# Kernel optimization log

Measured on AMD Instinct MI355X. Metric: run time of the kernel, lower is better.

Reference implementation:

```python
import jax, jax.numpy as jnp
import numpy as np
from jax import lax

K = 3          # dcn kernel size
KK = K * K     # 9 taps
PAD = 1


def _conv(x, w, b, pad):
    y = lax.conv_general_dilated(
        x, w, window_strides=(1, 1), padding=[(pad, pad), (pad, pad)],
        dimension_numbers=("NCHW", "OIHW", "NCHW"))
    return y + b[None, :, None, None]


def _bilinear_gather(x, py, px):
    """Zero-padded bilinear sampling.
    x: [B,C,Hin,Win]; py,px: [B,KK,H,W] float sample coords.
    returns [B,C,KK,H,W]."""
    B, C, Hin, Win = x.shape
    y0 = jnp.floor(py)
    x0 = jnp.floor(px)
    ly = py - y0   # frac weights
    lx = px - x0
    xf = x.reshape(B, C, Hin * Win)

    def corner(yc, xc, w):
        valid = (yc >= 0) & (yc <= Hin - 1) & (xc >= 0) & (xc <= Win - 1)
        yi = jnp.clip(yc, 0, Hin - 1).astype(jnp.int32)
        xi = jnp.clip(xc, 0, Win - 1).astype(jnp.int32)
        idx = yi * Win + xi                              # [B,KK,H,W]
        vals = jax.vmap(lambda f, i: jnp.take(f, i, axis=1))(xf, idx)  # [B,C,KK,H,W]
        return vals * (w * valid.astype(x.dtype))[:, None]

    out = corner(y0,     x0,     (1 - ly) * (1 - lx))
    out = out + corner(y0,     x0 + 1, (1 - ly) * lx)
    out = out + corner(y0 + 1, x0,     ly * (1 - lx))
    out = out + corner(y0 + 1, x0 + 1, ly * lx)
    return out


def _forward(x, conv1_w, conv1_b, off_w, off_b, dcn_w, dcn_b):
    # features: Conv2d(1,3,3,s1,p1) + ReLU + MaxPool(3,2)
    h = jax.nn.relu(_conv(x, conv1_w, conv1_b, pad=1))
    h = lax.reduce_window(h, -jnp.inf, lax.max,
                          window_dimensions=(1, 1, 3, 3),
                          window_strides=(1, 1, 2, 2), padding="VALID")
    B, C, H, W = h.shape

    # DCNv2: conv_offset_mask -> (dy, dx, sigmoid mask)
    om = _conv(h, off_w, off_b, pad=PAD)          # [B, 3*KK, H, W]
    dy = om[:, :KK]
    dx = om[:, KK:2 * KK]
    mask = jax.nn.sigmoid(om[:, 2 * KK:])         # [B, KK, H, W]

    # base sampling grid (stride 1, pad 1, dilation 1)
    ky = (jnp.arange(KK) // K).astype(h.dtype)    # kernel row of each tap
    kx = (jnp.arange(KK) % K).astype(h.dtype)
    hh = jnp.arange(H, dtype=h.dtype)
    ww = jnp.arange(W, dtype=h.dtype)
    py = hh[None, None, :, None] - PAD + ky[None, :, None, None] + dy
    px = ww[None, None, None, :] - PAD + kx[None, :, None, None] + dx

    sampled = _bilinear_gather(h, py, px)          # [B,C,KK,H,W]
    sampled = sampled * mask[:, None]              # modulation
    out = jnp.einsum("bckhw,ock->bohw", sampled,
                     dcn_w.reshape(dcn_w.shape[0], C, KK))
    return out + dcn_b[None, :, None, None]


def setup_inputs() -> dict:
    key = jax.random.key(0)
    ks = jax.random.split(key, 7)
    x = jax.random.normal(ks[0], (32, 1, 512, 512), dtype=jnp.float32)
    conv1_w = jax.random.normal(ks[1], (3, 1, 3, 3), dtype=jnp.float32) * 0.5
    conv1_b = jnp.zeros((3,), dtype=jnp.float32)
    # offset/mask conv: 3*KK = 27 output channels; small init so offsets are modest
    off_w = jax.random.normal(ks[2], (3 * KK, 3, 3, 3), dtype=jnp.float32) * 0.01
    off_b = jax.random.normal(ks[3], (3 * KK,), dtype=jnp.float32) * 0.01
    dcn_w = jax.random.normal(ks[4], (3, 3, 3, 3), dtype=jnp.float32) * 0.1
    dcn_b = jnp.zeros((3,), dtype=jnp.float32)
    return {"x": x, "conv1_w": conv1_w, "conv1_b": conv1_b,
            "off_w": off_w, "off_b": off_b, "dcn_w": dcn_w, "dcn_b": dcn_b}


def reference(x, conv1_w, conv1_b, off_w, off_b, dcn_w, dcn_b):
    return _forward(x, conv1_w, conv1_b, off_w, off_b, dcn_w, dcn_b)
```

## Files before the change

### kernel.cpp

```cpp
#include <hip/hip_runtime.h>
#include <math.h>

#define B_  32
#define H0  512
#define W0  512
#define Hh  255
#define Wh  255
#define HP  259

typedef __attribute__((ext_vector_type(8))) short    bf16x8;
typedef __attribute__((ext_vector_type(4))) float    f32x4;
typedef __attribute__((ext_vector_type(4))) unsigned int u32x4;

static __device__ __forceinline__ unsigned int f2bf(float f) {
    unsigned int u = __float_as_uint(f);
    return (u + 0x7FFFu + ((u >> 16) & 1u)) >> 16;
}
static __device__ __forceinline__ float bflo(unsigned int u) { return __uint_as_float(u << 16); }
static __device__ __forceinline__ float bfhi(unsigned int u) { return __uint_as_float(u & 0xFFFF0000u); }

__global__ __launch_bounds__(256) void conv_pool_kernel(
    const float* __restrict__ x,
    const float* __restrict__ w,
    const float* __restrict__ bias,
    uint2* __restrict__ hp)
{
    __shared__ float sx[35][36];
    __shared__ float sc[33 * 100];
    const int b  = blockIdx.z;
    const int i0 = blockIdx.y * 16;
    const int j0 = blockIdx.x * 16;
    const int tx = threadIdx.x, ty = threadIdx.y;
    const int tid = ty * 16 + tx;

    const float* xb = x + b * (H0 * W0);
    for (int t = tid; t < 35 * 35; t += 256) {
        int r = t / 35, c = t - r * 35;
        int gr = 2 * i0 - 1 + r;
        int gc = 2 * j0 - 1 + c;
        float v = 0.f;
        if ((unsigned)gr < (unsigned)H0 && (unsigned)gc < (unsigned)W0) v = xb[gr * W0 + gc];
        sx[r][c] = v;
    }
    __syncthreads();

    float w0[9], w1[9], w2[9];
#pragma unroll
    for (int t = 0; t < 9; ++t) { w0[t] = w[t]; w1[t] = w[9 + t]; w2[t] = w[18 + t]; }
    const float b0 = bias[0], b1 = bias[1], b2 = bias[2];

    for (int t = tid; t < 33 * 33; t += 256) {
        int r = t / 33, c = t - r * 33;
        float s0 = b0, s1 = b1, s2 = b2;
#pragma unroll
        for (int ky = 0; ky < 3; ++ky) {
#pragma unroll
            for (int kx = 0; kx < 3; ++kx) {
                float v = sx[r + ky][c + kx];
                s0 = fmaf(w0[ky * 3 + kx], v, s0);
                s1 = fmaf(w1[ky * 3 + kx], v, s1);
                s2 = fmaf(w2[ky * 3 + kx], v, s2);
            }
        }
        float* p = &sc[r * 100 + c * 3];
        p[0] = s0; p[1] = s1; p[2] = s2;
    }
    __syncthreads();

    const int i = i0 + ty, j = j0 + tx;
    if (i >= Hh || j >= Wh) return;

    float m0 = -1e30f, m1 = -1e30f, m2 = -1e30f;
#pragma unroll
    for (int pr = 0; pr < 3; ++pr) {
#pragma unroll
        for (int pc = 0; pc < 3; ++pc) {
            const float* p = &sc[(2 * ty + pr) * 100 + (2 * tx + pc) * 3];
            m0 = fmaxf(m0, p[0]);
            m1 = fmaxf(m1, p[1]);
            m2 = fmaxf(m2, p[2]);
        }
    }
    m0 = fmaxf(m0, 0.f); m1 = fmaxf(m1, 0.f); m2 = fmaxf(m2, 0.f);

    uint2 v;
    v.x = f2bf(m0) | (f2bf(m1) << 16);
    v.y = f2bf(m2);
    hp[(b * HP + i + 2) * HP + (j + 2)] = v;
}

__global__ __launch_bounds__(256, 5) void dcn_kernel(
    const uint2* __restrict__ hp,
    const float* __restrict__ off_w,
    const float* __restrict__ off_b,
    const float* __restrict__ dcn_w,
    const float* __restrict__ dcn_b,
    float* __restrict__ out)
{
    __shared__ __align__(16) char smem[256 * 28 * 4];
    float* om_s = (float*)smem;

    const int y   = blockIdx.x;
    const int b   = blockIdx.y;
    const int tid = threadIdx.x;
    const int x   = tid;

    const uint2* hb = hp + b * (HP * HP);

    {
        unsigned short* Bm = (unsigned short*)(smem + 16384);
        for (int idx = tid; idx < 1024; idx += 256) {
            int n = idx >> 5, k = idx & 31;
            float v = (n < 27 && k < 27) ? off_w[n * 27 + k] : 0.f;
            Bm[n * 32 + k] = (unsigned short)f2bf(v);
        }
    }

    unsigned int L[9], Hv[9];
#pragma unroll
    for (int ky = 0; ky < 3; ++ky) {
        const unsigned int rbase = (unsigned int)(y + 1 + ky) * HP + (unsigned int)(x + 1);
#pragma unroll
        for (int kx = 0; kx < 3; ++kx) {
            uint2 v = hb[rbase + kx];
            L[ky * 3 + kx]  = v.x;
            Hv[ky * 3 + kx] = v.y;
        }
    }

    {
        unsigned int T[16];
        T[0]  = (L[0] & 0xFFFFu) | (L[1] << 16);
        T[1]  = (L[2] & 0xFFFFu) | (L[3] << 16);
        T[2]  = (L[4] & 0xFFFFu) | (L[5] << 16);
        T[3]  = (L[6] & 0xFFFFu) | (L[7] << 16);
        T[4]  = (L[8] & 0xFFFFu) | (L[0] & 0xFFFF0000u);
        T[5]  = (L[1] >> 16) | (L[2] & 0xFFFF0000u);
        T[6]  = (L[3] >> 16) | (L[4] & 0xFFFF0000u);
        T[7]  = (L[5] >> 16) | (L[6] & 0xFFFF0000u);
        T[8]  = (L[7] >> 16) | (L[8] & 0xFFFF0000u);
        T[9]  = (Hv[0] & 0xFFFFu) | (Hv[1] << 16);
        T[10] = (Hv[2] & 0xFFFFu) | (Hv[3] << 16);
        T[11] = (Hv[4] & 0xFFFFu) | (Hv[5] << 16);
        T[12] = (Hv[6] & 0xFFFFu) | (Hv[7] << 16);
        T[13] = (Hv[8] & 0xFFFFu);
        T[14] = 0u;
        T[15] = 0u;
#pragma unroll
        for (int c4 = 0; c4 < 4; ++c4) {
            u32x4 v = { T[c4 * 4 + 0], T[c4 * 4 + 1], T[c4 * 4 + 2], T[c4 * 4 + 3] };
            *(u32x4*)(smem + (c4 * 256 + tid) * 16) = v;
        }
    }
    __syncthreads();

    {
        const int wave = tid >> 6, lane = tid & 63;
        const int lrow = lane & 15, lchunk = lane >> 4;
        const short* As = (const short*)smem;
        const short* Bs = (const short*)(smem + 16384);

        bf16x8 afr[4];
#pragma unroll
        for (int m = 0; m < 4; ++m)
            afr[m] = *(const bf16x8*)(As + (lchunk * 256 + wave * 64 + m * 16 + lrow) * 8);
        bf16x8 bfr[2];
#pragma unroll
        for (int nt = 0; nt < 2; ++nt)
            bfr[nt] = *(const bf16x8*)(Bs + ((nt * 16 + lrow) * 32 + lchunk * 8));

        f32x4 acc[4][2];
#pragma unroll
        for (int m = 0; m < 4; ++m)
#pragma unroll
            for (int nt = 0; nt < 2; ++nt) {
                f32x4 z = {0.f, 0.f, 0.f, 0.f};
                acc[m][nt] = __builtin_amdgcn_mfma_f32_16x16x32_bf16(afr[m], bfr[nt], z, 0, 0, 0);
            }
        __syncthreads();

#pragma unroll
        for (int m = 0; m < 4; ++m)
#pragma unroll
            for (int nt = 0; nt < 2; ++nt) {
                const int n = nt * 16 + lrow;
                if (n < 27) {
                    const int pxb = wave * 64 + m * 16 + lchunk * 4;
                    om_s[(pxb + 0) * 28 + n] = acc[m][nt][0];
                    om_s[(pxb + 1) * 28 + n] = acc[m][nt][1];
                    om_s[(pxb + 2) * 28 + n] = acc[m][nt][2];
                    om_s[(pxb + 3) * 28 + n] = acc[m][nt][3];
                }
            }
    }
    __syncthreads();

    f32x4 o4[7];
    {
        const f32x4* omv = (const f32x4*)(om_s + x * 28);
#pragma unroll
        for (int j = 0; j < 7; ++j) o4[j] = omv[j];
    }

    float outv0 = dcn_b[0], outv1 = dcn_b[1], outv2 = dcn_b[2];
    const float yf = (float)y, xf = (float)x;

#pragma unroll
    for (int k = 0; k < 9; ++k) {
        const float dy  = o4[k >> 2][k & 3]               + off_b[k];
        const float dxx = o4[(k + 9) >> 2][(k + 9) & 3]   + off_b[9 + k];
        const float zm  = o4[(k + 18) >> 2][(k + 18) & 3] + off_b[18 + k];
        const float msk = __builtin_amdgcn_rcpf(1.f + __expf(-zm));

        const float py = yf + (float)(k / 3 - 1) + dy;
        const float px = xf + (float)(k % 3 - 1) + dxx;

        const float y0f = floorf(py), x0f = floorf(px);
        const float ly = py - y0f, lx = px - x0f;
        int iy = (int)y0f, ix = (int)x0f;
        iy = min(max(iy, -2), 255);
        ix = min(max(ix, -2), 255);

        const unsigned int idx = (unsigned int)(iy + 2) * HP + (unsigned int)(ix + 2);
        const uint2 aAA = hb[idx];
        const uint2 aAB = hb[idx + 1];
        const uint2 aBA = hb[idx + HP];
        const uint2 aBB = hb[idx + HP + 1];

        const float my1 = ly * msk;
        const float my0 = msk - my1;
        const float lx1 = 1.f - lx;
        const float w00 = my0 * lx1, w01 = my0 * lx;
        const float w10 = my1 * lx1, w11 = my1 * lx;

        const float s0 = w00 * bflo(aAA.x) + w01 * bflo(aAB.x) + w10 * bflo(aBA.x) + w11 * bflo(aBB.x);
        const float s1 = w00 * bfhi(aAA.x) + w01 * bfhi(aAB.x) + w10 * bfhi(aBA.x) + w11 * bfhi(aBB.x);
        const float s2 = w00 * bflo(aAA.y) + w01 * bflo(aAB.y) + w10 * bflo(aBA.y) + w11 * bflo(aBB.y);

        outv0 = fmaf(dcn_w[0 * 27 + 0 * 9 + k], s0, outv0);
        outv0 = fmaf(dcn_w[0 * 27 + 1 * 9 + k], s1, outv0);
        outv0 = fmaf(dcn_w[0 * 27 + 2 * 9 + k], s2, outv0);
        outv1 = fmaf(dcn_w[1 * 27 + 0 * 9 + k], s0, outv1);
        outv1 = fmaf(dcn_w[1 * 27 + 1 * 9 + k], s1, outv1);
        outv1 = fmaf(dcn_w[1 * 27 + 2 * 9 + k], s2, outv1);
        outv2 = fmaf(dcn_w[2 * 27 + 0 * 9 + k], s0, outv2);
        outv2 = fmaf(dcn_w[2 * 27 + 1 * 9 + k], s1, outv2);
        outv2 = fmaf(dcn_w[2 * 27 + 2 * 9 + k], s2, outv2);
    }

    if (x < Wh) {
        const int hwsz = Hh * Wh;
        const int o = (b * 3) * hwsz + y * Wh + x;
        out[o]            = outv0;
        out[o + hwsz]     = outv1;
        out[o + 2 * hwsz] = outv2;
    }
}

extern "C" void kernel_launch(void* const* d_in, const int* in_sizes, int n_in,
                              void* d_out, int out_size, void* d_ws, size_t ws_size,
                              hipStream_t stream) {
    const float* x       = (const float*)d_in[0];
    const float* conv1_w = (const float*)d_in[1];
    const float* conv1_b = (const float*)d_in[2];
    const float* off_w   = (const float*)d_in[3];
    const float* off_b   = (const float*)d_in[4];
    const float* dcn_w   = (const float*)d_in[5];
    const float* dcn_b   = (const float*)d_in[6];
    float* out = (float*)d_out;
    uint2* hp  = (uint2*)d_ws;

    hipMemsetAsync(d_ws, 0, (size_t)B_ * HP * HP * sizeof(uint2), stream);

    conv_pool_kernel<<<dim3(16, 16, B_), dim3(16, 16), 0, stream>>>(x, conv1_w, conv1_b, hp);
    dcn_kernel<<<dim3(Hh, B_), 256, 0, stream>>>(hp, off_w, off_b, dcn_w, dcn_b, out);
}
```

Before: 81.51 us.

## Replace full workspace memset with border-only zeroing, fold bias into MFMA, vectorize gathers

Removes the full-buffer hipMemsetAsync and instead zeroes only the two-pixel padding ring of the pooled feature map, using an extra row of blocks in the conv/pool kernel. The offset-conv bias is folded into the MFMA by adding a constant-1 input column and a bias row in the weight tile. The four corner loads of the bilinear sampling become two 16-byte loads, and the pooling max is rewritten as a flat expression. The border-only zeroing depends on every interior cell being written by conv_pool on each call, and the bias now passes through bf16 rounding.

```diff
diff --git a/kernel.cpp b/kernel.cpp
--- a/kernel.cpp
+++ b/kernel.cpp
@@ -25,13 +25,32 @@
     const float* __restrict__ bias,
     uint2* __restrict__ hp)
 {
+    const int b = blockIdx.z;
+    const int tx = threadIdx.x, ty = threadIdx.y;
+    const int tid = ty * 16 + tx;
+
+    if (blockIdx.y == 16) {
+        uint2* hpb = hp + b * (HP * HP);
+        const int gid = blockIdx.x * 256 + tid;
+        if (gid < 2072) {
+            int r, c;
+            if (gid < 1036) {
+                int rr = gid / 259; c = gid - rr * 259;
+                r = rr + (rr >= 2 ? 255 : 0);
+            } else {
+                int u = gid - 1036;
+                int cc = u / 259; r = u - cc * 259;
+                c = cc + (cc >= 2 ? 255 : 0);
+            }
+            hpb[r * HP + c] = make_uint2(0u, 0u);
+        }
+        return;
+    }
+
     __shared__ float sx[35][36];
     __shared__ float sc[33 * 100];
-    const int b  = blockIdx.z;
     const int i0 = blockIdx.y * 16;
     const int j0 = blockIdx.x * 16;
-    const int tx = threadIdx.x, ty = threadIdx.y;
-    const int tid = ty * 16 + tx;
 
     const float* xb = x + b * (H0 * W0);
     for (int t = tid; t < 35 * 35; t += 256) {
@@ -70,17 +89,13 @@
     const int i = i0 + ty, j = j0 + tx;
     if (i >= Hh || j >= Wh) return;
 
-    float m0 = -1e30f, m1 = -1e30f, m2 = -1e30f;
-#pragma unroll
-    for (int pr = 0; pr < 3; ++pr) {
-#pragma unroll
-        for (int pc = 0; pc < 3; ++pc) {
-            const float* p = &sc[(2 * ty + pr) * 100 + (2 * tx + pc) * 3];
-            m0 = fmaxf(m0, p[0]);
-            m1 = fmaxf(m1, p[1]);
-            m2 = fmaxf(m2, p[2]);
-        }
-    }
+    const float* r0 = &sc[(2 * ty + 0) * 100 + (2 * tx) * 3];
+    const float* r1 = &sc[(2 * ty + 1) * 100 + (2 * tx) * 3];
+    const float* r2 = &sc[(2 * ty + 2) * 100 + (2 * tx) * 3];
+#define MAX3_(a, bq, cq) fmaxf(fmaxf((a), (bq)), (cq))
+    float m0 = MAX3_(MAX3_(r0[0], r0[3], r0[6]), MAX3_(r1[0], r1[3], r1[6]), MAX3_(r2[0], r2[3], r2[6]));
+    float m1 = MAX3_(MAX3_(r0[1], r0[4], r0[7]), MAX3_(r1[1], r1[4], r1[7]), MAX3_(r2[1], r2[4], r2[7]));
+    float m2 = MAX3_(MAX3_(r0[2], r0[5], r0[8]), MAX3_(r1[2], r1[5], r1[8]), MAX3_(r2[2], r2[5], r2[8]));
     m0 = fmaxf(m0, 0.f); m1 = fmaxf(m1, 0.f); m2 = fmaxf(m2, 0.f);
 
     uint2 v;
@@ -111,7 +126,8 @@
         unsigned short* Bm = (unsigned short*)(smem + 16384);
         for (int idx = tid; idx < 1024; idx += 256) {
             int n = idx >> 5, k = idx & 31;
-            float v = (n < 27 && k < 27) ? off_w[n * 27 + k] : 0.f;
+            float v = 0.f;
+            if (n < 27) { if (k < 27) v = off_w[n * 27 + k]; else if (k == 27) v = off_b[n]; }
             Bm[n * 32 + k] = (unsigned short)f2bf(v);
         }
     }
@@ -143,7 +159,7 @@
         T[10] = (Hv[2] & 0xFFFFu) | (Hv[3] << 16);
         T[11] = (Hv[4] & 0xFFFFu) | (Hv[5] << 16);
         T[12] = (Hv[6] & 0xFFFFu) | (Hv[7] << 16);
-        T[13] = (Hv[8] & 0xFFFFu);
+        T[13] = (Hv[8] & 0xFFFFu) | 0x3F800000u;
         T[14] = 0u;
         T[15] = 0u;
 #pragma unroll
@@ -207,9 +223,9 @@
 
 #pragma unroll
     for (int k = 0; k < 9; ++k) {
-        const float dy  = o4[k >> 2][k & 3]               + off_b[k];
-        const float dxx = o4[(k + 9) >> 2][(k + 9) & 3]   + off_b[9 + k];
-        const float zm  = o4[(k + 18) >> 2][(k + 18) & 3] + off_b[18 + k];
+        const float dy  = o4[k >> 2][k & 3];
+        const float dxx = o4[(k + 9) >> 2][(k + 9) & 3];
+        const float zm  = o4[(k + 18) >> 2][(k + 18) & 3];
         const float msk = __builtin_amdgcn_rcpf(1.f + __expf(-zm));
 
         const float py = yf + (float)(k / 3 - 1) + dy;
@@ -217,15 +233,14 @@
 
         const float y0f = floorf(py), x0f = floorf(px);
         const float ly = py - y0f, lx = px - x0f;
-        int iy = (int)y0f, ix = (int)x0f;
-        iy = min(max(iy, -2), 255);
-        ix = min(max(ix, -2), 255);
-
-        const unsigned int idx = (unsigned int)(iy + 2) * HP + (unsigned int)(ix + 2);
-        const uint2 aAA = hb[idx];
-        const uint2 aAB = hb[idx + 1];
-        const uint2 aBA = hb[idx + HP];
-        const uint2 aBB = hb[idx + HP + 1];
+        int iy = (int)y0f + 2, ix = (int)x0f + 2;
+        iy = min(max(iy, 0), 257);
+        ix = min(max(ix, 0), 257);
+
+        const unsigned int idx = (unsigned int)iy * HP + (unsigned int)ix;
+        u32x4 ua, ub;
+        __builtin_memcpy(&ua, hb + idx, 16);
+        __builtin_memcpy(&ub, hb + idx + HP, 16);
 
         const float my1 = ly * msk;
         const float my0 = msk - my1;
@@ -233,9 +248,9 @@
         const float w00 = my0 * lx1, w01 = my0 * lx;
         const float w10 = my1 * lx1, w11 = my1 * lx;
 
-        const float s0 = w00 * bflo(aAA.x) + w01 * bflo(aAB.x) + w10 * bflo(aBA.x) + w11 * bflo(aBB.x);
-        const float s1 = w00 * bfhi(aAA.x) + w01 * bfhi(aAB.x) + w10 * bfhi(aBA.x) + w11 * bfhi(aBB.x);
-        const float s2 = w00 * bflo(aAA.y) + w01 * bflo(aAB.y) + w10 * bflo(aBA.y) + w11 * bflo(aBB.y);
+        const float s0 = w00 * bflo(ua.x) + w01 * bflo(ua.z) + w10 * bflo(ub.x) + w11 * bflo(ub.z);
+        const float s1 = w00 * bfhi(ua.x) + w01 * bfhi(ua.z) + w10 * bfhi(ub.x) + w11 * bfhi(ub.z);
+        const float s2 = w00 * bflo(ua.y) + w01 * bflo(ua.w) + w10 * bflo(ub.y) + w11 * bflo(ub.w);
 
         outv0 = fmaf(dcn_w[0 * 27 + 0 * 9 + k], s0, outv0);
         outv0 = fmaf(dcn_w[0 * 27 + 1 * 9 + k], s1, outv0);
@@ -270,8 +285,6 @@
     float* out = (float*)d_out;
     uint2* hp  = (uint2*)d_ws;
 
-    hipMemsetAsync(d_ws, 0, (size_t)B_ * HP * HP * sizeof(uint2), stream);
-
-    conv_pool_kernel<<<dim3(16, 16, B_), dim3(16, 16), 0, stream>>>(x, conv1_w, conv1_b, hp);
+    conv_pool_kernel<<<dim3(16, 17, B_), dim3(16, 16), 0, stream>>>(x, conv1_w, conv1_b, hp);
     dcn_kernel<<<dim3(Hh, B_), 256, 0, stream>>>(hp, off_w, off_b, dcn_w, dcn_b, out);
 }
```

Result: faster. 71.67 us (-12.1%).
